# Kernel optimization log

Hardware: AMD Instinct MI355X
Metric: run time of the kernel (lower is better)

The kernel has to match this reference:

```python
import jax, jax.numpy as jnp
import numpy as np

T, B, C = 1024, 8, 1024
H, K, P = 16, 7, 3  # num_heads, kernel_size, padding_l
R = C // H


def setup_inputs() -> dict:
    key = jax.random.key(0)
    k1, k2, k3, k4 = jax.random.split(key, 4)
    x = jax.random.normal(k1, (T, B, C), dtype=jnp.float32)
    # weight_linear: Linear(C -> H*K) with bias
    lim = 1.0 / np.sqrt(C)
    W_lin = jax.random.uniform(k2, (H * K, C), minval=-lim, maxval=lim, dtype=jnp.float32)
    b_lin = jax.random.uniform(k3, (H * K,), minval=-lim, maxval=lim, dtype=jnp.float32)
    conv_bias = jnp.zeros((C,), dtype=jnp.float32)
    return {"x": x, "W_lin": W_lin, "b_lin": b_lin, "conv_bias": conv_bias}


def reference(x, W_lin, b_lin, conv_bias):
    # per-position dynamic filters: (T, B, H*K)
    w = jnp.einsum('tbc,oc->tbo', x, W_lin) + b_lin
    # weight_softmax=True, renorm_padding=False: softmax over kernel dim
    w = jax.nn.softmax(w.reshape(T * B * H, K), axis=-1)
    # (T, B*H, K) -> (B*H, T, K)
    w = w.reshape(T, B * H, K).transpose(1, 0, 2)
    # x as (B*H, T, R)
    xv = x.reshape(T, B * H, R).transpose(1, 0, 2)
    # band-matrix bmm == sliding window: out[t] = sum_k w[t,k] * x[t - P + k]
    x_pad = jnp.pad(xv, ((0, 0), (P, K - 1 - P), (0, 0)))
    windows = jnp.stack([x_pad[:, k:k + T] for k in range(K)], axis=2)  # (BH, T, K, R)
    out = jnp.einsum('btk,btkr->btr', w, windows)  # (BH, T, R)
    out = out.transpose(1, 0, 2).reshape(T, B, C)
    return out + conv_bias[None, None, :]
```

## Files before the change

### kernel.cpp

```cpp
#include <hip/hip_runtime.h>
#include <stdint.h>

#define T_DIM 1024
#define B_DIM 8
#define C_DIM 1024
#define H_DIM 16
#define K_SZ  7
#define P_PAD 3
#define O_DIM (H_DIM * K_SZ)
#define TB    (T_DIM * B_DIM)

typedef __attribute__((ext_vector_type(8))) short bf16x8;
typedef __attribute__((ext_vector_type(4))) float f32x4;
typedef __attribute__((ext_vector_type(4))) uint32_t u32x4;

union FragU { uint32_t u[4]; bf16x8 v; };

__device__ inline uint32_t pk_bf16(float a, float b) {
  uint32_t ua = __float_as_uint(a), ub = __float_as_uint(b);
  ua += 0x7FFFu + ((ua >> 16) & 1u);
  ub += 0x7FFFu + ((ub >> 16) & 1u);
  return (ua >> 16) | (ub & 0xFFFF0000u);
}

__device__ inline bf16x8 load_bf16x8_cvt(const float* __restrict__ p) {
  float4 lo = *reinterpret_cast<const float4*>(p);
  float4 hi = *reinterpret_cast<const float4*>(p + 4);
  FragU f;
  f.u[0] = pk_bf16(lo.x, lo.y);
  f.u[1] = pk_bf16(lo.z, lo.w);
  f.u[2] = pk_bf16(hi.x, hi.y);
  f.u[3] = pk_bf16(hi.z, hi.w);
  return f.v;
}

__global__ __launch_bounds__(256) void prep_wfrag_kernel(
    const float* __restrict__ Wl, uint16_t* __restrict__ Wf) {
  const int t  = blockIdx.x * 256 + threadIdx.x;
  const int f  = t >> 6;
  const int l  = t & 63;
  const int ks = f / 7;
  const int nf = f - ks * 7;
  const int row = nf * 16 + (l & 15);
  const int kb  = ks * 32 + (l >> 4) * 8;
  bf16x8 v = load_bf16x8_cvt(Wl + (size_t)row * C_DIM + kb);
  *reinterpret_cast<bf16x8*>(Wf + (size_t)t * 8) = v;
}

template <bool PREPPED>
__global__ __launch_bounds__(512) void fused_dynconv_kernel(
    const float* __restrict__ x, const float* __restrict__ Wl,
    const uint16_t* __restrict__ Wf, const float* __restrict__ bl,
    const float* __restrict__ cb, float* __restrict__ out) {
  __shared__ char  xbf[22 * 2048];
  __shared__ float part[2][16][116];
  __shared__ float wsm[16][17][8];

  const int tid  = threadIdx.x;
  const int wv   = tid >> 6;
  const int lane = tid & 63;
  const int l15  = lane & 15;
  const int oct  = lane >> 4;

  const int bid    = blockIdx.x;
  const int w8     = bid >> 3;
  const int t_tile = (bid & 7) * 8 + (w8 & 7);
  const int b      = w8 >> 3;
  const int t0     = t_tile * 16;

  {
#pragma unroll
    for (int it = 0; it < 6; ++it) {
      const int task = tid + it * 512;
      if (task < 22 * 128) {
        const int q    = task >> 7;
        const int c16  = task & 127;
        const int trow = min(max(t0 + q - P_PAD, 0), T_DIM - 1);
        const float* __restrict__ src =
            x + ((size_t)(trow * B_DIM + b)) * C_DIM + c16 * 8;
        float4 v0 = *reinterpret_cast<const float4*>(src);
        float4 v1 = *reinterpret_cast<const float4*>(src + 4);
        FragU f;
        f.u[0] = pk_bf16(v0.x, v0.y);
        f.u[1] = pk_bf16(v0.z, v0.w);
        f.u[2] = pk_bf16(v1.x, v1.y);
        f.u[3] = pk_bf16(v1.z, v1.w);
        const int dst = q * 2048 + ((c16 * 16) ^ ((q & 7) << 4));
        *reinterpret_cast<bf16x8*>(xbf + dst) = f.v;
      }
    }
  }
  __syncthreads();

  {
    const int kh  = wv >> 2;
    const int nfq = wv & 3;
    const int nf0 = nfq * 2;
    const int nfc = (nfq == 3) ? 1 : 2;
    f32x4 acc0 = (f32x4)(0.f), acc1 = (f32x4)(0.f);
    const int arow  = 3 + l15;
    const int abase = arow * 2048;
    const int axor  = (arow & 7) << 4;
#pragma unroll
    for (int s = 0; s < 16; ++s) {
      const int ksg = kh * 16 + s;
      bf16x8 a = *reinterpret_cast<const bf16x8*>(
          xbf + abase + ((ksg * 64 + oct * 16) ^ axor));
      bf16x8 b0, b1;
      if (PREPPED) {
        b0 = *reinterpret_cast<const bf16x8*>(
            Wf + ((size_t)((ksg * 7 + nf0) * 64) + lane) * 8);
        if (nfc == 2)
          b1 = *reinterpret_cast<const bf16x8*>(
              Wf + ((size_t)((ksg * 7 + nf0 + 1) * 64) + lane) * 8);
      } else {
        b0 = load_bf16x8_cvt(Wl + (size_t)(nf0 * 16 + l15) * C_DIM + ksg * 32 + oct * 8);
        if (nfc == 2)
          b1 = load_bf16x8_cvt(Wl + (size_t)((nf0 + 1) * 16 + l15) * C_DIM + ksg * 32 + oct * 8);
      }
      acc0 = __builtin_amdgcn_mfma_f32_16x16x32_bf16(a, b0, acc0, 0, 0, 0);
      if (nfc == 2)
        acc1 = __builtin_amdgcn_mfma_f32_16x16x32_bf16(a, b1, acc1, 0, 0, 0);
    }
#pragma unroll
    for (int r = 0; r < 4; ++r)
      part[kh][oct * 4 + r][nf0 * 16 + l15] = acc0[r];
    if (nfc == 2) {
#pragma unroll
      for (int r = 0; r < 4; ++r)
        part[kh][oct * 4 + r][(nf0 + 1) * 16 + l15] = acc1[r];
    }
  }
  __syncthreads();

  if (tid < 256) {
    const int row = tid >> 4;
    const int h   = tid & 15;
    float lg[7];
    float m = -1e30f;
#pragma unroll
    for (int j = 0; j < 7; ++j) {
      const int c = h * 7 + j;
      float s_ = part[0][row][c] + part[1][row][c] + bl[c];
      lg[j] = s_;
      m = fmaxf(m, s_);
    }
    float s = 0.f;
#pragma unroll
    for (int j = 0; j < 7; ++j) { lg[j] = __expf(lg[j] - m); s += lg[j]; }
    const float inv = 1.0f / s;
#pragma unroll
    for (int j = 0; j < 7; ++j) wsm[row][h][j] = lg[j] * inv;
  }
  __syncthreads();

  {
    const int row   = tid >> 5;
    const int t32   = tid & 31;
    const int tglob = t0 + row;
    float okf[7];
#pragma unroll
    for (int j = 0; j < 7; ++j) {
      int tp = tglob + j - P_PAD;
      okf[j] = (tp >= 0 && tp < T_DIM) ? 1.f : 0.f;
    }
    float* __restrict__ obase = out + ((size_t)(tglob * B_DIM + b)) * C_DIM;

#pragma unroll
    for (int ii = 0; ii < 4; ++ii) {
      const int ch0  = ii * 256 + t32 * 8;
      const int head = ch0 >> 6;
      float4 w0 = *reinterpret_cast<const float4*>(&wsm[row][head][0]);
      float4 w1 = *reinterpret_cast<const float4*>(&wsm[row][head][4]);
      const float wj[7] = {w0.x, w0.y, w0.z, w0.w, w1.x, w1.y, w1.z};
      float4 c0 = *reinterpret_cast<const float4*>(cb + ch0);
      float4 c1 = *reinterpret_cast<const float4*>(cb + ch0 + 4);
      float a0 = c0.x, a1 = c0.y, a2 = c0.z, a3 = c0.w;
      float a4 = c1.x, a5 = c1.y, a6 = c1.z, a7 = c1.w;
#pragma unroll
      for (int j = 0; j < 7; ++j) {
        const float w = wj[j] * okf[j];
        const int q = row + j;
        const u32x4 d = *reinterpret_cast<const u32x4*>(
            xbf + q * 2048 + ((ch0 * 2) ^ ((q & 7) << 4)));
        a0 += w * __uint_as_float(d.x << 16);
        a1 += w * __uint_as_float(d.x & 0xffff0000u);
        a2 += w * __uint_as_float(d.y << 16);
        a3 += w * __uint_as_float(d.y & 0xffff0000u);
        a4 += w * __uint_as_float(d.z << 16);
        a5 += w * __uint_as_float(d.z & 0xffff0000u);
        a6 += w * __uint_as_float(d.w << 16);
        a7 += w * __uint_as_float(d.w & 0xffff0000u);
      }
      *reinterpret_cast<float4*>(obase + ch0)     = make_float4(a0, a1, a2, a3);
      *reinterpret_cast<float4*>(obase + ch0 + 4) = make_float4(a4, a5, a6, a7);
    }
  }
}

extern "C" void kernel_launch(void* const* d_in, const int* in_sizes, int n_in,
                              void* d_out, int out_size, void* d_ws, size_t ws_size,
                              hipStream_t stream) {
  const float* x  = (const float*)d_in[0];
  const float* Wl = (const float*)d_in[1];
  const float* bl = (const float*)d_in[2];
  const float* cb = (const float*)d_in[3];
  float* out = (float*)d_out;

  const bool prepped = ws_size >= 262144;

  if (prepped) {
    uint16_t* wf = (uint16_t*)d_ws;
    prep_wfrag_kernel<<<(32 * 7 * 64) / 256, 256, 0, stream>>>(Wl, wf);
    fused_dynconv_kernel<true><<<TB / 16, 512, 0, stream>>>(x, Wl, wf, bl, cb, out);
  } else {
    fused_dynconv_kernel<false><<<TB / 16, 512, 0, stream>>>(x, Wl, nullptr, bl, cb, out);
  }
}
```

Baseline: 30.21 us.

## Process two time tiles per block with ring buffer and register prefetch

Each block now handles 32 time steps as two 16-row sub-tiles using 1024 threads and a 32-slot LDS ring, so the 6-row halo is loaded once instead of twice. The second tile's x rows are prefetched into registers before the first tile's MFMA/softmax/conv phases and written into the ring afterward, overlapping global loads with compute. The grid drops to 256 blocks with 14 waves doing MFMA, which reduces parallelism and may leave CUs underused. Barriers are replaced with raw s_barrier plus an lgkmcnt wait.

After: 29.67 us. Within noise of the previous version (-1.8%).

```diff
diff --git a/kernel.cpp b/kernel.cpp
--- a/kernel.cpp
+++ b/kernel.cpp
@@ -32,6 +32,13 @@
   f.u[2] = pk_bf16(hi.x, hi.y);
   f.u[3] = pk_bf16(hi.z, hi.w);
   return f.v;
+}
+
+__device__ inline void bar_lds() {
+  __builtin_amdgcn_sched_barrier(0);
+  asm volatile("s_waitcnt lgkmcnt(0)" ::: "memory");
+  __builtin_amdgcn_s_barrier();
+  __builtin_amdgcn_sched_barrier(0);
 }
 
 __global__ __launch_bounds__(256) void prep_wfrag_kernel(
@@ -48,11 +55,11 @@
 }
 
 template <bool PREPPED>
-__global__ __launch_bounds__(512) void fused_dynconv_kernel(
+__global__ __launch_bounds__(1024, 4) void fused_pipe_kernel(
     const float* __restrict__ x, const float* __restrict__ Wl,
     const uint16_t* __restrict__ Wf, const float* __restrict__ bl,
     const float* __restrict__ cb, float* __restrict__ out) {
-  __shared__ char  xbf[22 * 2048];
+  __shared__ char  ring[32 * 2048];
   __shared__ float part[2][16][116];
   __shared__ float wsm[16][17][8];
 
@@ -62,113 +69,95 @@
   const int l15  = lane & 15;
   const int oct  = lane >> 4;
 
-  const int bid    = blockIdx.x;
-  const int w8     = bid >> 3;
-  const int t_tile = (bid & 7) * 8 + (w8 & 7);
-  const int b      = w8 >> 3;
-  const int t0     = t_tile * 16;
-
-  {
-#pragma unroll
-    for (int it = 0; it < 6; ++it) {
-      const int task = tid + it * 512;
-      if (task < 22 * 128) {
-        const int q    = task >> 7;
-        const int c16  = task & 127;
-        const int trow = min(max(t0 + q - P_PAD, 0), T_DIM - 1);
-        const float* __restrict__ src =
-            x + ((size_t)(trow * B_DIM + b)) * C_DIM + c16 * 8;
-        float4 v0 = *reinterpret_cast<const float4*>(src);
-        float4 v1 = *reinterpret_cast<const float4*>(src + 4);
-        FragU f;
-        f.u[0] = pk_bf16(v0.x, v0.y);
-        f.u[1] = pk_bf16(v0.z, v0.w);
-        f.u[2] = pk_bf16(v1.x, v1.y);
-        f.u[3] = pk_bf16(v1.z, v1.w);
-        const int dst = q * 2048 + ((c16 * 16) ^ ((q & 7) << 4));
-        *reinterpret_cast<bf16x8*>(xbf + dst) = f.v;
+  const int bid = blockIdx.x;
+  const int xcd = bid & 7;
+  const int r8  = bid >> 3;
+  const int b   = r8 >> 2;
+  const int t0  = (xcd * 4 + (r8 & 3)) * 32;
+
+  auto stage_write = [&](int task, int gbase) {
+    const int q   = task >> 7;
+    const int c16 = task & 127;
+    const int g   = min(max(gbase + q, 0), T_DIM - 1);
+    const float* __restrict__ src =
+        x + ((size_t)(g * B_DIM + b)) * C_DIM + c16 * 8;
+    float4 v0 = *reinterpret_cast<const float4*>(src);
+    float4 v1 = *reinterpret_cast<const float4*>(src + 4);
+    FragU f;
+    f.u[0] = pk_bf16(v0.x, v0.y);
+    f.u[1] = pk_bf16(v0.z, v0.w);
+    f.u[2] = pk_bf16(v1.x, v1.y);
+    f.u[3] = pk_bf16(v1.z, v1.w);
+    const int dst = (g & 31) * 2048 + ((c16 * 16) ^ ((g & 7) << 4));
+    *reinterpret_cast<bf16x8*>(ring + dst) = f.v;
+  };
+
+  auto mfma_phase = [&](int wbase) {
+    if (wv < 14) {
+      const int kh = (wv >= 7) ? 1 : 0;
+      const int nf = wv - kh * 7;
+      f32x4 acc = (f32x4)(0.f);
+      const int ag   = wbase + l15;
+      const char* ab = ring + (ag & 31) * 2048;
+      const int axor = (ag & 7) << 4;
+#pragma unroll
+      for (int s = 0; s < 16; ++s) {
+        const int ksg = kh * 16 + s;
+        bf16x8 a = *reinterpret_cast<const bf16x8*>(
+            ab + ((ksg * 64 + oct * 16) ^ axor));
+        bf16x8 bf;
+        if (PREPPED)
+          bf = *reinterpret_cast<const bf16x8*>(
+              Wf + ((size_t)((ksg * 7 + nf) * 64) + lane) * 8);
+        else
+          bf = load_bf16x8_cvt(Wl + (size_t)(nf * 16 + l15) * C_DIM + ksg * 32 + oct * 8);
+        acc = __builtin_amdgcn_mfma_f32_16x16x32_bf16(a, bf, acc, 0, 0, 0);
       }
-    }
-  }
-  __syncthreads();
-
-  {
-    const int kh  = wv >> 2;
-    const int nfq = wv & 3;
-    const int nf0 = nfq * 2;
-    const int nfc = (nfq == 3) ? 1 : 2;
-    f32x4 acc0 = (f32x4)(0.f), acc1 = (f32x4)(0.f);
-    const int arow  = 3 + l15;
-    const int abase = arow * 2048;
-    const int axor  = (arow & 7) << 4;
-#pragma unroll
-    for (int s = 0; s < 16; ++s) {
-      const int ksg = kh * 16 + s;
-      bf16x8 a = *reinterpret_cast<const bf16x8*>(
-          xbf + abase + ((ksg * 64 + oct * 16) ^ axor));
-      bf16x8 b0, b1;
-      if (PREPPED) {
-        b0 = *reinterpret_cast<const bf16x8*>(
-            Wf + ((size_t)((ksg * 7 + nf0) * 64) + lane) * 8);
-        if (nfc == 2)
-          b1 = *reinterpret_cast<const bf16x8*>(
-              Wf + ((size_t)((ksg * 7 + nf0 + 1) * 64) + lane) * 8);
-      } else {
-        b0 = load_bf16x8_cvt(Wl + (size_t)(nf0 * 16 + l15) * C_DIM + ksg * 32 + oct * 8);
-        if (nfc == 2)
-          b1 = load_bf16x8_cvt(Wl + (size_t)((nf0 + 1) * 16 + l15) * C_DIM + ksg * 32 + oct * 8);
+#pragma unroll
+      for (int rr = 0; rr < 4; ++rr)
+        part[kh][oct * 4 + rr][nf * 16 + l15] = acc[rr];
+    }
+  };
+
+  auto softmax_phase = [&]() {
+    if (tid < 256) {
+      const int row = tid >> 4;
+      const int h   = tid & 15;
+      float lg[7];
+      float m = -1e30f;
+#pragma unroll
+      for (int j = 0; j < 7; ++j) {
+        const int c = h * 7 + j;
+        float s_ = part[0][row][c] + part[1][row][c] + bl[c];
+        lg[j] = s_;
+        m = fmaxf(m, s_);
       }
-      acc0 = __builtin_amdgcn_mfma_f32_16x16x32_bf16(a, b0, acc0, 0, 0, 0);
-      if (nfc == 2)
-        acc1 = __builtin_amdgcn_mfma_f32_16x16x32_bf16(a, b1, acc1, 0, 0, 0);
-    }
-#pragma unroll
-    for (int r = 0; r < 4; ++r)
-      part[kh][oct * 4 + r][nf0 * 16 + l15] = acc0[r];
-    if (nfc == 2) {
-#pragma unroll
-      for (int r = 0; r < 4; ++r)
-        part[kh][oct * 4 + r][(nf0 + 1) * 16 + l15] = acc1[r];
-    }
-  }
-  __syncthreads();
-
-  if (tid < 256) {
-    const int row = tid >> 4;
-    const int h   = tid & 15;
-    float lg[7];
-    float m = -1e30f;
+      float s = 0.f;
+#pragma unroll
+      for (int j = 0; j < 7; ++j) { lg[j] = __expf(lg[j] - m); s += lg[j]; }
+      const float inv = 1.0f / s;
+#pragma unroll
+      for (int j = 0; j < 7; ++j) wsm[row][h][j] = lg[j] * inv;
+    }
+  };
+
+  auto conv_phase = [&](int wbase) {
+    const int row  = wv;
+    const int gout = wbase + row;
+    float okf[7];
+    int slotb[7], sxor[7];
 #pragma unroll
     for (int j = 0; j < 7; ++j) {
-      const int c = h * 7 + j;
-      float s_ = part[0][row][c] + part[1][row][c] + bl[c];
-      lg[j] = s_;
-      m = fmaxf(m, s_);
-    }
-    float s = 0.f;
-#pragma unroll
-    for (int j = 0; j < 7; ++j) { lg[j] = __expf(lg[j] - m); s += lg[j]; }
-    const float inv = 1.0f / s;
-#pragma unroll
-    for (int j = 0; j < 7; ++j) wsm[row][h][j] = lg[j] * inv;
-  }
-  __syncthreads();
-
-  {
-    const int row   = tid >> 5;
-    const int t32   = tid & 31;
-    const int tglob = t0 + row;
-    float okf[7];
-#pragma unroll
-    for (int j = 0; j < 7; ++j) {
-      int tp = tglob + j - P_PAD;
+      const int tp = gout + j - P_PAD;
       okf[j] = (tp >= 0 && tp < T_DIM) ? 1.f : 0.f;
-    }
-    float* __restrict__ obase = out + ((size_t)(tglob * B_DIM + b)) * C_DIM;
-
-#pragma unroll
-    for (int ii = 0; ii < 4; ++ii) {
-      const int ch0  = ii * 256 + t32 * 8;
+      const int g = min(max(tp, 0), T_DIM - 1);
+      slotb[j] = (g & 31) * 2048;
+      sxor[j]  = (g & 7) << 4;
+    }
+    float* __restrict__ obase = out + ((size_t)(gout * B_DIM + b)) * C_DIM;
+#pragma unroll
+    for (int ii = 0; ii < 2; ++ii) {
+      const int ch0  = ii * 512 + lane * 8;
       const int head = ch0 >> 6;
       float4 w0 = *reinterpret_cast<const float4*>(&wsm[row][head][0]);
       float4 w1 = *reinterpret_cast<const float4*>(&wsm[row][head][4]);
@@ -180,9 +169,8 @@
 #pragma unroll
       for (int j = 0; j < 7; ++j) {
         const float w = wj[j] * okf[j];
-        const int q = row + j;
         const u32x4 d = *reinterpret_cast<const u32x4*>(
-            xbf + q * 2048 + ((ch0 * 2) ^ ((q & 7) << 4)));
+            ring + slotb[j] + ((ch0 * 2) ^ sxor[j]));
         a0 += w * __uint_as_float(d.x << 16);
         a1 += w * __uint_as_float(d.x & 0xffff0000u);
         a2 += w * __uint_as_float(d.y << 16);
@@ -195,7 +183,67 @@
       *reinterpret_cast<float4*>(obase + ch0)     = make_float4(a0, a1, a2, a3);
       *reinterpret_cast<float4*>(obase + ch0 + 4) = make_float4(a4, a5, a6, a7);
     }
-  }
+  };
+
+#pragma unroll
+  for (int it = 0; it < 3; ++it) {
+    const int task = tid + it * 1024;
+    if (task < 22 * 128) stage_write(task, t0 - 3);
+  }
+  bar_lds();
+
+  float4 pf0, pf1, pf2, pf3;
+  {
+    const int q0 = tid >> 7, c0_ = tid & 127;
+    const int g0 = min(t0 + 19 + q0, T_DIM - 1);
+    const float* __restrict__ s0 =
+        x + ((size_t)(g0 * B_DIM + b)) * C_DIM + c0_ * 8;
+    pf0 = *reinterpret_cast<const float4*>(s0);
+    pf1 = *reinterpret_cast<const float4*>(s0 + 4);
+    const int t2 = tid + 1024;
+    const int q1 = t2 >> 7, c1_ = t2 & 127;
+    const int g1 = min(t0 + 19 + q1, T_DIM - 1);
+    const float* __restrict__ s1 =
+        x + ((size_t)(g1 * B_DIM + b)) * C_DIM + c1_ * 8;
+    pf2 = *reinterpret_cast<const float4*>(s1);
+    pf3 = *reinterpret_cast<const float4*>(s1 + 4);
+  }
+
+  mfma_phase(t0);
+  bar_lds();
+  softmax_phase();
+  bar_lds();
+  conv_phase(t0);
+  bar_lds();
+
+  {
+    const int q0 = tid >> 7, c0_ = tid & 127;
+    const int g0 = min(t0 + 19 + q0, T_DIM - 1);
+    FragU f;
+    f.u[0] = pk_bf16(pf0.x, pf0.y);
+    f.u[1] = pk_bf16(pf0.z, pf0.w);
+    f.u[2] = pk_bf16(pf1.x, pf1.y);
+    f.u[3] = pk_bf16(pf1.z, pf1.w);
+    *reinterpret_cast<bf16x8*>(
+        ring + (g0 & 31) * 2048 + ((c0_ * 16) ^ ((g0 & 7) << 4))) = f.v;
+    const int t2 = tid + 1024;
+    const int q1 = t2 >> 7, c1_ = t2 & 127;
+    const int g1 = min(t0 + 19 + q1, T_DIM - 1);
+    FragU f2;
+    f2.u[0] = pk_bf16(pf2.x, pf2.y);
+    f2.u[1] = pk_bf16(pf2.z, pf2.w);
+    f2.u[2] = pk_bf16(pf3.x, pf3.y);
+    f2.u[3] = pk_bf16(pf3.z, pf3.w);
+    *reinterpret_cast<bf16x8*>(
+        ring + (g1 & 31) * 2048 + ((c1_ * 16) ^ ((g1 & 7) << 4))) = f2.v;
+  }
+  bar_lds();
+
+  mfma_phase(t0 + 16);
+  bar_lds();
+  softmax_phase();
+  bar_lds();
+  conv_phase(t0 + 16);
 }
 
 extern "C" void kernel_launch(void* const* d_in, const int* in_sizes, int n_in,
@@ -212,8 +260,8 @@
   if (prepped) {
     uint16_t* wf = (uint16_t*)d_ws;
     prep_wfrag_kernel<<<(32 * 7 * 64) / 256, 256, 0, stream>>>(Wl, wf);
-    fused_dynconv_kernel<true><<<TB / 16, 512, 0, stream>>>(x, Wl, wf, bl, cb, out);
+    fused_pipe_kernel<true><<<256, 1024, 0, stream>>>(x, Wl, wf, bl, cb, out);
   } else {
-    fused_dynconv_kernel<false><<<TB / 16, 512, 0, stream>>>(x, Wl, nullptr, bl, cb, out);
-  }
-}
+    fused_pipe_kernel<false><<<256, 1024, 0, stream>>>(x, Wl, nullptr, bl, cb, out);
+  }
+}
```
